# Kernel optimization log

Measured on AMD Instinct MI355X. Metric: run time of the kernel, lower is better.

The kernel has to match this reference:

```python
import jax, jax.numpy as jnp
import numpy as np

B, N, E, DIN, H1, H2, DOUT = 2, 20000, 320000, 128, 256, 256, 128


def setup_inputs() -> dict:
    key = jax.random.key(0)
    ks = jax.random.split(key, 9)
    X = jax.random.normal(ks[0], (B, N, DIN), dtype=jnp.float32)
    edge_index = jax.random.randint(ks[1], (2, E), 0, N, dtype=jnp.int32)
    def lin(k, fan_in, fan_out):
        lim = 1.0 / np.sqrt(fan_in)
        return jax.random.uniform(k, (fan_in, fan_out), jnp.float32, -lim, lim)
    W1 = lin(ks[2], DIN, H1); b1 = jnp.zeros((H1,), jnp.float32)
    W2 = lin(ks[3], H1, H2);  b2 = jnp.zeros((H2,), jnp.float32)
    W3 = lin(ks[4], H2, DOUT); b3 = jnp.zeros((DOUT,), jnp.float32)
    prelu_a = jnp.array(0.25, jnp.float32)  # PReLU default single shared param
    return dict(X=X, W1=W1, b1=b1, W2=W2, b2=b2, W3=W3, b3=b3,
                prelu_a=prelu_a, edge_index=edge_index)


def reference(X, W1, b1, W2, b2, W3, b3, prelu_a, edge_index):
    src, dst = edge_index[0], edge_index[1]
    n = X.shape[1]
    # GCN symmetric normalization with self-loops: deg = in-degree + 1
    deg = jax.ops.segment_sum(jnp.ones_like(src, X.dtype), dst, num_segments=n) + 1.0
    dinv = jax.lax.rsqrt(deg)                      # [N]
    norm_e = dinv[src] * dinv[dst]                 # [E] edge norm
    norm_self = dinv * dinv                        # [N] self-loop norm

    def gcn(x, W, b):
        h = x @ W                                  # [N, F_out]
        agg = jax.ops.segment_sum(h[src] * norm_e[:, None], dst, num_segments=n)
        agg = agg + h * norm_self[:, None]         # add self-loop message
        return agg + b

    def prelu(x):
        return jnp.where(x >= 0, x, prelu_a * x)

    def single(x):  # x: [N, DIN]
        x = prelu(gcn(x, W1, b1))
        x = prelu(gcn(x, W2, b2))
        return gcn(x, W3, b3)

    return jax.vmap(single)(X)                     # [B, N, DOUT]
```

## Files before the change

kernel.cpp:

```cpp
#include <hip/hip_runtime.h>

#define NB 20000
#define EB 320000
#define DIN 128
#define H1D 256
#define H2D 256
#define DOUTD 128
#define SCAN_BLOCKS ((NB + 255) / 256)


__global__ void zero_kernel(int* __restrict__ p, int n) {
    int t = blockIdx.x * blockDim.x + threadIdx.x;
    if (t < n) p[t] = 0;
}

__global__ void hist_kernel(const int* __restrict__ dst, int* __restrict__ bins) {
    int t = blockIdx.x * blockDim.x + threadIdx.x;
    if (t < EB) atomicAdd(&bins[dst[t]], 1);
}

__global__ __launch_bounds__(256) void scanA_kernel(const int* __restrict__ bins,
                                                    int* __restrict__ loc,
                                                    int* __restrict__ blksum) {
    __shared__ int s[256];
    int t = threadIdx.x;
    int i = blockIdx.x * 256 + t;
    int v = (i < NB) ? bins[i] : 0;
    s[t] = v;
    __syncthreads();
    for (int off = 1; off < 256; off <<= 1) {
        int u = (t >= off) ? s[t - off] : 0;
        __syncthreads();
        s[t] += u;
        __syncthreads();
    }
    if (i < NB) loc[i] = s[t] - v;
    if (t == 255) blksum[blockIdx.x] = s[255];
}

__global__ __launch_bounds__(128) void scanB_kernel(int* __restrict__ blksum) {
    __shared__ int s[128];
    int t = threadIdx.x;
    int v = (t < SCAN_BLOCKS) ? blksum[t] : 0;
    s[t] = v;
    __syncthreads();
    for (int off = 1; off < 128; off <<= 1) {
        int u = (t >= off) ? s[t - off] : 0;
        __syncthreads();
        s[t] += u;
        __syncthreads();
    }
    if (t < SCAN_BLOCKS) blksum[t] = s[t] - v;
}

__global__ __launch_bounds__(256) void scanC_kernel(const int* __restrict__ bins,
                                                    const int* __restrict__ loc,
                                                    const int* __restrict__ blksum,
                                                    int* __restrict__ rs,
                                                    int* __restrict__ cursor,
                                                    float* __restrict__ dinv) {
    int i = blockIdx.x * 256 + threadIdx.x;
    if (i < NB) {
        int r = loc[i] + blksum[blockIdx.x];
        rs[i] = r;
        cursor[i] = r;
        dinv[i] = rsqrtf((float)bins[i] + 1.0f);
    }
    if (i == 0) rs[NB] = EB;
}

__global__ void scatter_kernel(const int* __restrict__ src, const int* __restrict__ dst,
                               const float* __restrict__ dinv,
                               int* __restrict__ cursor, int2* __restrict__ edges) {
    int t = blockIdx.x * blockDim.x + threadIdx.x;
    if (t < EB) {
        int d = dst[t], s = src[t];
        int p = atomicAdd(&cursor[d], 1);
        edges[p] = make_int2(s, __float_as_int(dinv[s] * dinv[d]));
    }
}


template <int F, bool SPLIT_IN, bool SPLIT_OUT, bool BIAS, bool PRELU>
__global__ __launch_bounds__(256) void aggv_kernel(
    const float* __restrict__ h, float* __restrict__ out,
    const int* __restrict__ rs, const int2* __restrict__ edges,
    const float* __restrict__ dinv, const float* __restrict__ bias,
    const float* __restrict__ pa, int phase) {
    const int ss = blockIdx.x & 7;
    const int chunk = blockIdx.x >> 3;
    const int wid = threadIdx.x >> 6;
    const int lane = threadIdx.x & 63;
    const int li = lane & 31;
    const int eh = lane >> 5;
    const int b = ss >> 2;
    const int c32 = (ss & 3) + phase * 4;
    const int fo = c32 * 32 + li;

    constexpr size_t GS = SPLIT_IN ? F : 2 * F;
    constexpr size_t OS = SPLIT_OUT ? F : 2 * F;
    const float* gb = h + (SPLIT_IN ? (size_t)b * NB * F : (size_t)b * F) + fo;
    float* ob = out + (SPLIT_OUT ? (size_t)b * NB * F : (size_t)b * F) + fo;

    const float pav = PRELU ? *pa : 0.0f;
    const float bval = BIAS ? bias[fo] : 0.0f;

    int n = chunk * 20 + wid * 5;
    int e1n = __builtin_amdgcn_readfirstlane(rs[n]);
    for (int j = 0; j < 5; ++j, ++n) {
        int e0 = e1n;
        e1n = __builtin_amdgcn_readfirstlane(rs[n + 1]);
        int e1 = e1n;
        float a0 = 0.f, a1 = 0.f, a2 = 0.f, a3 = 0.f;
        int e = e0;
        for (; e + 8 <= e1; e += 8) {
            int2 r0 = edges[e + eh];
            int2 r1 = edges[e + 2 + eh];
            int2 r2 = edges[e + 4 + eh];
            int2 r3 = edges[e + 6 + eh];
            float t0 = gb[(size_t)r0.x * GS];
            float t1 = gb[(size_t)r1.x * GS];
            float t2 = gb[(size_t)r2.x * GS];
            float t3 = gb[(size_t)r3.x * GS];
            a0 = fmaf(t0, __int_as_float(r0.y), a0);
            a1 = fmaf(t1, __int_as_float(r1.y), a1);
            a2 = fmaf(t2, __int_as_float(r2.y), a2);
            a3 = fmaf(t3, __int_as_float(r3.y), a3);
        }
        for (; e + 2 <= e1; e += 2) {
            int2 r0 = edges[e + eh];
            a0 = fmaf(gb[(size_t)r0.x * GS], __int_as_float(r0.y), a0);
        }
        if (e < e1) {
            int my = e + eh;
            bool valid = (my < e1);
            int2 r0 = edges[valid ? my : e];
            float w = valid ? __int_as_float(r0.y) : 0.0f;
            a0 = fmaf(gb[(size_t)r0.x * GS], w, a0);
        }
        float acc = (a0 + a1) + (a2 + a3);
        acc += __shfl_xor(acc, 32, 64);
        float dv = dinv[n];
        float r = fmaf(gb[(size_t)n * GS], dv * dv, acc);
        if (BIAS) r += bval;
        if (PRELU) r = (r >= 0.0f) ? r : pav * r;
        if (eh == 0) ob[(size_t)n * OS] = r;
    }
}

template <bool BIAS, bool PRELU>
__global__ __launch_bounds__(256) void gemm_kernel(const float* __restrict__ A, int M, int K,
                                                   const float* __restrict__ W, int Nc,
                                                   const float* __restrict__ bias,
                                                   const float* __restrict__ pa,
                                                   float* __restrict__ C) {
    __shared__ alignas(16) float As[16][132];
    __shared__ alignas(16) float Bs[16][68];
    int t = threadIdx.x;
    int bm = blockIdx.x * 128;
    int bn = blockIdx.y * 64;
    int tx = t & 15, ty = t >> 4;
    int m0 = ty * 8, n0 = tx * 4;
    int ar = t >> 2, ac4 = (t & 3) * 4;
    int br = t >> 4, bc4 = (t & 15) * 4;

    float acc[8][4] = {};

    for (int k0 = 0; k0 < K; k0 += 16) {
        float4 a0 = make_float4(0.f, 0.f, 0.f, 0.f), a1 = a0;
        int r0 = bm + ar, r1 = bm + ar + 64;
        if (r0 < M) a0 = *(const float4*)&A[(size_t)r0 * K + k0 + ac4];
        if (r1 < M) a1 = *(const float4*)&A[(size_t)r1 * K + k0 + ac4];
        As[ac4 + 0][ar] = a0.x; As[ac4 + 1][ar] = a0.y;
        As[ac4 + 2][ar] = a0.z; As[ac4 + 3][ar] = a0.w;
        As[ac4 + 0][ar + 64] = a1.x; As[ac4 + 1][ar + 64] = a1.y;
        As[ac4 + 2][ar + 64] = a1.z; As[ac4 + 3][ar + 64] = a1.w;
        float4 bv = *(const float4*)&W[(size_t)(k0 + br) * Nc + bn + bc4];
        *(float4*)&Bs[br][bc4] = bv;
        __syncthreads();
#pragma unroll
        for (int k = 0; k < 16; ++k) {
            float4 av0 = *(const float4*)&As[k][m0];
            float4 av1 = *(const float4*)&As[k][m0 + 4];
            float4 bv4 = *(const float4*)&Bs[k][n0];
            float a_[8] = {av0.x, av0.y, av0.z, av0.w, av1.x, av1.y, av1.z, av1.w};
            float b_[4] = {bv4.x, bv4.y, bv4.z, bv4.w};
#pragma unroll
            for (int i = 0; i < 8; ++i)
#pragma unroll
                for (int j = 0; j < 4; ++j)
                    acc[i][j] = fmaf(a_[i], b_[j], acc[i][j]);
        }
        __syncthreads();
    }

    float pav = 0.0f;
    if (PRELU) pav = *pa;
#pragma unroll
    for (int i = 0; i < 8; ++i) {
        int row = bm + m0 + i;
        if (row < M) {
            float v[4];
#pragma unroll
            for (int j = 0; j < 4; ++j) {
                float x = acc[i][j];
                if (BIAS) x += bias[bn + n0 + j];
                if (PRELU) x = (x >= 0.0f) ? x : pav * x;
                v[j] = x;
            }
            *(float4*)&C[(size_t)row * Nc + bn + n0] = make_float4(v[0], v[1], v[2], v[3]);
        }
    }
}


static inline char* carve(char*& p, size_t bytes) {
    char* r = p;
    p += (bytes + 255) & ~(size_t)255;
    return r;
}

extern "C" void kernel_launch(void* const* d_in, const int* in_sizes, int n_in,
                              void* d_out, int out_size, void* d_ws, size_t ws_size,
                              hipStream_t stream) {
    const float* X  = (const float*)d_in[0];
    const float* W1 = (const float*)d_in[1];
    const float* b1 = (const float*)d_in[2];
    const float* W2 = (const float*)d_in[3];
    const float* b2 = (const float*)d_in[4];
    const float* W3 = (const float*)d_in[5];
    const float* b3 = (const float*)d_in[6];
    const float* pa = (const float*)d_in[7];
    const int* ei   = (const int*)d_in[8];
    const int* src = ei;
    const int* dst = ei + EB;
    float* out = (float*)d_out;

    char* p = (char*)d_ws;
    int* bins    = (int*)carve(p, NB * sizeof(int));
    int* loc     = (int*)carve(p, NB * sizeof(int));
    int* blksum  = (int*)carve(p, 128 * sizeof(int));
    int* rs      = (int*)carve(p, (NB + 1) * sizeof(int));
    int* cursor  = (int*)carve(p, NB * sizeof(int));
    int2* edges  = (int2*)carve(p, EB * sizeof(int2));
    float* dinv  = (float*)carve(p, NB * sizeof(float));
    float* bufA  = (float*)carve(p, (size_t)2 * NB * 256 * sizeof(float));
    float* bufB  = (float*)carve(p, (size_t)2 * NB * 256 * sizeof(float));

    const int M = 2 * NB;
    const int AGGV = 1000 * 8;

    zero_kernel<<<SCAN_BLOCKS, 256, 0, stream>>>(bins, NB);
    hist_kernel<<<(EB + 255) / 256, 256, 0, stream>>>(dst, bins);
    scanA_kernel<<<SCAN_BLOCKS, 256, 0, stream>>>(bins, loc, blksum);
    scanB_kernel<<<1, 128, 0, stream>>>(blksum);
    scanC_kernel<<<SCAN_BLOCKS, 256, 0, stream>>>(bins, loc, blksum, rs, cursor, dinv);
    scatter_kernel<<<(EB + 255) / 256, 256, 0, stream>>>(src, dst, dinv, cursor, edges);

    aggv_kernel<128, true, false, false, false><<<AGGV, 256, 0, stream>>>(
        X, bufA, rs, edges, dinv, nullptr, nullptr, 0);

    gemm_kernel<true, true><<<dim3((M + 127) / 128, H1D / 64), 256, 0, stream>>>(
        bufA, M, DIN, W1, H1D, b1, pa, bufB);

    gemm_kernel<false, false><<<dim3((M + 127) / 128, H2D / 64), 256, 0, stream>>>(
        bufB, M, H1D, W2, H2D, nullptr, nullptr, bufA);

    aggv_kernel<256, false, false, true, true><<<AGGV, 256, 0, stream>>>(
        bufA, bufB, rs, edges, dinv, b2, pa, 0);
    aggv_kernel<256, false, false, true, true><<<AGGV, 256, 0, stream>>>(
        bufA, bufB, rs, edges, dinv, b2, pa, 1);

    gemm_kernel<false, false><<<dim3((M + 127) / 128, DOUTD / 64), 256, 0, stream>>>(
        bufB, M, H2D, W3, DOUTD, nullptr, nullptr, bufA);

    aggv_kernel<128, false, true, true, false><<<AGGV, 256, 0, stream>>>(
        bufA, out, rs, edges, dinv, b3, nullptr, 0);
}
```

Baseline: 490.7 us.

## Pipeline the two batches so GEMM and aggregation blocks share launches

Splits the two batch elements into separate per-batch buffers and staggers them. Each launch then runs the GEMM tiles of one batch alongside the sparse aggregation blocks of the other, so compute-bound and gather-bound work overlap. The GEMM also gains register prefetch of the next k-tile and nontemporal loads and stores in the fused variant. This adds launch-level complexity and depends on how the hardware scheduler interleaves the heterogeneous blocks. Block dispatch order could still leave either side as a tail.

```diff
diff --git a/kernel.cpp b/kernel.cpp
--- a/kernel.cpp
+++ b/kernel.cpp
@@ -7,6 +7,27 @@
 #define H2D 256
 #define DOUTD 128
 #define SCAN_BLOCKS ((NB + 255) / 256)
+#define MT 157
+
+typedef __attribute__((ext_vector_type(4))) float fvec4;
+
+template <bool NT>
+__device__ inline float4 ld4(const float* p) {
+    if (NT) {
+        fvec4 v = __builtin_nontemporal_load((const fvec4*)p);
+        return make_float4(v.x, v.y, v.z, v.w);
+    }
+    return *(const float4*)p;
+}
+template <bool NT>
+__device__ inline void st4(float* p, float4 v) {
+    if (NT) {
+        fvec4 t; t.x = v.x; t.y = v.y; t.z = v.z; t.w = v.w;
+        __builtin_nontemporal_store(t, (fvec4*)p);
+    } else {
+        *(float4*)p = v;
+    }
+}
 
 
 __global__ void zero_kernel(int* __restrict__ p, int n) {
@@ -81,31 +102,29 @@
 }
 
 
-template <int F, bool SPLIT_IN, bool SPLIT_OUT, bool BIAS, bool PRELU>
-__global__ __launch_bounds__(256) void aggv_kernel(
-    const float* __restrict__ h, float* __restrict__ out,
-    const int* __restrict__ rs, const int2* __restrict__ edges,
-    const float* __restrict__ dinv, const float* __restrict__ bias,
-    const float* __restrict__ pa, int phase) {
-    const int ss = blockIdx.x & 7;
-    const int chunk = blockIdx.x >> 3;
+template <int F, bool BIAS, bool PRELU>
+__device__ void aggv_body(int a, int ss,
+                          const float* __restrict__ h, float* __restrict__ out,
+                          const int* __restrict__ rs, const int2* __restrict__ edges,
+                          const float* __restrict__ dinv, const float* __restrict__ bias,
+                          const float* __restrict__ pa) {
+    constexpr int NS = F / 32;
+    constexpr int NH = 8 / NS;
+    const int half = (NH == 2) ? (ss >> 2) : 0;
+    const int c32 = ss & (NS - 1);
+    const int chunk = a >> 3;
     const int wid = threadIdx.x >> 6;
     const int lane = threadIdx.x & 63;
     const int li = lane & 31;
     const int eh = lane >> 5;
-    const int b = ss >> 2;
-    const int c32 = (ss & 3) + phase * 4;
     const int fo = c32 * 32 + li;
 
-    constexpr size_t GS = SPLIT_IN ? F : 2 * F;
-    constexpr size_t OS = SPLIT_OUT ? F : 2 * F;
-    const float* gb = h + (SPLIT_IN ? (size_t)b * NB * F : (size_t)b * F) + fo;
-    float* ob = out + (SPLIT_OUT ? (size_t)b * NB * F : (size_t)b * F) + fo;
-
+    const float* gb = h + fo;
+    float* ob = out + fo;
     const float pav = PRELU ? *pa : 0.0f;
     const float bval = BIAS ? bias[fo] : 0.0f;
 
-    int n = chunk * 20 + wid * 5;
+    int n = half * (NB / NH) + chunk * 20 + wid * 5;
     int e1n = __builtin_amdgcn_readfirstlane(rs[n]);
     for (int j = 0; j < 5; ++j, ++n) {
         int e0 = e1n;
@@ -118,10 +137,10 @@
             int2 r1 = edges[e + 2 + eh];
             int2 r2 = edges[e + 4 + eh];
             int2 r3 = edges[e + 6 + eh];
-            float t0 = gb[(size_t)r0.x * GS];
-            float t1 = gb[(size_t)r1.x * GS];
-            float t2 = gb[(size_t)r2.x * GS];
-            float t3 = gb[(size_t)r3.x * GS];
+            float t0 = gb[(size_t)r0.x * F];
+            float t1 = gb[(size_t)r1.x * F];
+            float t2 = gb[(size_t)r2.x * F];
+            float t3 = gb[(size_t)r3.x * F];
             a0 = fmaf(t0, __int_as_float(r0.y), a0);
             a1 = fmaf(t1, __int_as_float(r1.y), a1);
             a2 = fmaf(t2, __int_as_float(r2.y), a2);
@@ -129,55 +148,65 @@
         }
         for (; e + 2 <= e1; e += 2) {
             int2 r0 = edges[e + eh];
-            a0 = fmaf(gb[(size_t)r0.x * GS], __int_as_float(r0.y), a0);
+            a0 = fmaf(gb[(size_t)r0.x * F], __int_as_float(r0.y), a0);
         }
         if (e < e1) {
             int my = e + eh;
             bool valid = (my < e1);
             int2 r0 = edges[valid ? my : e];
             float w = valid ? __int_as_float(r0.y) : 0.0f;
-            a0 = fmaf(gb[(size_t)r0.x * GS], w, a0);
+            a0 = fmaf(gb[(size_t)r0.x * F], w, a0);
         }
         float acc = (a0 + a1) + (a2 + a3);
         acc += __shfl_xor(acc, 32, 64);
         float dv = dinv[n];
-        float r = fmaf(gb[(size_t)n * GS], dv * dv, acc);
+        float r = fmaf(gb[(size_t)n * F], dv * dv, acc);
         if (BIAS) r += bval;
         if (PRELU) r = (r >= 0.0f) ? r : pav * r;
-        if (eh == 0) ob[(size_t)n * OS] = r;
-    }
-}
-
-template <bool BIAS, bool PRELU>
-__global__ __launch_bounds__(256) void gemm_kernel(const float* __restrict__ A, int M, int K,
-                                                   const float* __restrict__ W, int Nc,
-                                                   const float* __restrict__ bias,
-                                                   const float* __restrict__ pa,
-                                                   float* __restrict__ C) {
+        if (eh == 0) ob[(size_t)n * F] = r;
+    }
+}
+
+template <bool BIAS, bool PRELU, bool NT>
+__device__ void gemm_body(int gx, const float* __restrict__ A, int K,
+                          const float* __restrict__ W, int Nc,
+                          const float* __restrict__ bias, const float* __restrict__ pa,
+                          float* __restrict__ C) {
     __shared__ alignas(16) float As[16][132];
     __shared__ alignas(16) float Bs[16][68];
+    const int M = NB;
     int t = threadIdx.x;
-    int bm = blockIdx.x * 128;
-    int bn = blockIdx.y * 64;
+    int bm = (gx % MT) * 128;
+    int bn = (gx / MT) * 64;
     int tx = t & 15, ty = t >> 4;
     int m0 = ty * 8, n0 = tx * 4;
     int ar = t >> 2, ac4 = (t & 3) * 4;
     int br = t >> 4, bc4 = (t & 15) * 4;
+    int r0 = bm + ar, r1 = bm + ar + 64;
+    bool v0 = r0 < M, v1 = r1 < M;
+    const float* pA0 = A + (size_t)r0 * K + ac4;
+    const float* pA1 = A + (size_t)r1 * K + ac4;
+    const float* pW = W + (size_t)br * Nc + bn + bc4;
+
+    float4 a0 = make_float4(0.f, 0.f, 0.f, 0.f), a1 = a0;
+    if (v0) a0 = ld4<NT>(pA0);
+    if (v1) a1 = ld4<NT>(pA1);
+    float4 bv = *(const float4*)pW;
 
     float acc[8][4] = {};
 
     for (int k0 = 0; k0 < K; k0 += 16) {
-        float4 a0 = make_float4(0.f, 0.f, 0.f, 0.f), a1 = a0;
-        int r0 = bm + ar, r1 = bm + ar + 64;
-        if (r0 < M) a0 = *(const float4*)&A[(size_t)r0 * K + k0 + ac4];
-        if (r1 < M) a1 = *(const float4*)&A[(size_t)r1 * K + k0 + ac4];
         As[ac4 + 0][ar] = a0.x; As[ac4 + 1][ar] = a0.y;
         As[ac4 + 2][ar] = a0.z; As[ac4 + 3][ar] = a0.w;
         As[ac4 + 0][ar + 64] = a1.x; As[ac4 + 1][ar + 64] = a1.y;
         As[ac4 + 2][ar + 64] = a1.z; As[ac4 + 3][ar + 64] = a1.w;
-        float4 bv = *(const float4*)&W[(size_t)(k0 + br) * Nc + bn + bc4];
         *(float4*)&Bs[br][bc4] = bv;
         __syncthreads();
+        if (k0 + 16 < K) {
+            a0 = v0 ? ld4<NT>(pA0 + k0 + 16) : make_float4(0.f, 0.f, 0.f, 0.f);
+            a1 = v1 ? ld4<NT>(pA1 + k0 + 16) : make_float4(0.f, 0.f, 0.f, 0.f);
+            bv = *(const float4*)(pW + (size_t)(k0 + 16) * Nc);
+        }
 #pragma unroll
         for (int k = 0; k < 16; ++k) {
             float4 av0 = *(const float4*)&As[k][m0];
@@ -208,9 +237,48 @@
                 if (PRELU) x = (x >= 0.0f) ? x : pav * x;
                 v[j] = x;
             }
-            *(float4*)&C[(size_t)row * Nc + bn + n0] = make_float4(v[0], v[1], v[2], v[3]);
-        }
-    }
+            st4<NT>(&C[(size_t)row * Nc + bn + n0], make_float4(v[0], v[1], v[2], v[3]));
+        }
+    }
+}
+
+
+template <int F, bool BIAS, bool PRELU>
+__global__ __launch_bounds__(256) void aggv_kernel(
+    const float* __restrict__ h, float* __restrict__ out,
+    const int* __restrict__ rs, const int2* __restrict__ edges,
+    const float* __restrict__ dinv, const float* __restrict__ bias,
+    const float* __restrict__ pa) {
+    aggv_body<F, BIAS, PRELU>(blockIdx.x, blockIdx.x & 7, h, out, rs, edges,
+                              dinv, bias, pa);
+}
+
+template <int AF, bool AB, bool AP, bool GB_, bool GP>
+__global__ __launch_bounds__(256) void fat_kernel(
+    const float* __restrict__ A, int K, const float* __restrict__ W, int Nc,
+    const float* __restrict__ gbias, float* __restrict__ C, int ng,
+    const float* __restrict__ ah, float* __restrict__ aout,
+    const int* __restrict__ rs, const int2* __restrict__ edges,
+    const float* __restrict__ dinv, const float* __restrict__ abias,
+    const float* __restrict__ pa) {
+    int bx = blockIdx.x;
+    if (bx < ng) {
+        gemm_body<GB_, GP, true>(bx, A, K, W, Nc, gbias, pa, C);
+    } else {
+        aggv_body<AF, AB, AP>(bx - ng, bx & 7, ah, aout, rs, edges, dinv, abias, pa);
+    }
+}
+
+template <bool B1, bool P1, bool B2, bool P2>
+__global__ __launch_bounds__(256) void gemm2_kernel(
+    const float* __restrict__ A1p, int K1, const float* __restrict__ W1p, int N1,
+    const float* __restrict__ bias1, float* __restrict__ C1, int ng1,
+    const float* __restrict__ A2p, int K2, const float* __restrict__ W2p, int N2,
+    const float* __restrict__ bias2, float* __restrict__ C2,
+    const float* __restrict__ pa) {
+    int bx = blockIdx.x;
+    if (bx < ng1) gemm_body<B1, P1, false>(bx, A1p, K1, W1p, N1, bias1, pa, C1);
+    else          gemm_body<B2, P2, false>(bx - ng1, A2p, K2, W2p, N2, bias2, pa, C2);
 }
 
 
@@ -244,11 +312,15 @@
     int* cursor  = (int*)carve(p, NB * sizeof(int));
     int2* edges  = (int2*)carve(p, EB * sizeof(int2));
     float* dinv  = (float*)carve(p, NB * sizeof(float));
-    float* bufA  = (float*)carve(p, (size_t)2 * NB * 256 * sizeof(float));
-    float* bufB  = (float*)carve(p, (size_t)2 * NB * 256 * sizeof(float));
-
-    const int M = 2 * NB;
-    const int AGGV = 1000 * 8;
+    float* P0 = (float*)carve(p, (size_t)NB * 256 * sizeof(float));
+    float* Q0 = (float*)carve(p, (size_t)NB * 256 * sizeof(float));
+    float* P1 = (float*)carve(p, (size_t)NB * 256 * sizeof(float));
+    float* Q1 = (float*)carve(p, (size_t)NB * 256 * sizeof(float));
+
+    const float* X0 = X;
+    const float* X1 = X + (size_t)NB * DIN;
+    float* out0 = out;
+    float* out1 = out + (size_t)NB * DOUTD;
 
     zero_kernel<<<SCAN_BLOCKS, 256, 0, stream>>>(bins, NB);
     hist_kernel<<<(EB + 255) / 256, 256, 0, stream>>>(dst, bins);
@@ -257,23 +329,35 @@
     scanC_kernel<<<SCAN_BLOCKS, 256, 0, stream>>>(bins, loc, blksum, rs, cursor, dinv);
     scatter_kernel<<<(EB + 255) / 256, 256, 0, stream>>>(src, dst, dinv, cursor, edges);
 
-    aggv_kernel<128, true, false, false, false><<<AGGV, 256, 0, stream>>>(
-        X, bufA, rs, edges, dinv, nullptr, nullptr, 0);
-
-    gemm_kernel<true, true><<<dim3((M + 127) / 128, H1D / 64), 256, 0, stream>>>(
-        bufA, M, DIN, W1, H1D, b1, pa, bufB);
-
-    gemm_kernel<false, false><<<dim3((M + 127) / 128, H2D / 64), 256, 0, stream>>>(
-        bufB, M, H1D, W2, H2D, nullptr, nullptr, bufA);
-
-    aggv_kernel<256, false, false, true, true><<<AGGV, 256, 0, stream>>>(
-        bufA, bufB, rs, edges, dinv, b2, pa, 0);
-    aggv_kernel<256, false, false, true, true><<<AGGV, 256, 0, stream>>>(
-        bufA, bufB, rs, edges, dinv, b2, pa, 1);
-
-    gemm_kernel<false, false><<<dim3((M + 127) / 128, DOUTD / 64), 256, 0, stream>>>(
-        bufB, M, H2D, W3, DOUTD, nullptr, nullptr, bufA);
-
-    aggv_kernel<128, false, true, true, false><<<AGGV, 256, 0, stream>>>(
-        bufA, out, rs, edges, dinv, b3, nullptr, 0);
-}
+    const int NA128 = 4000;
+    const int NA256 = 8000;
+    const int NG256 = MT * 4;
+    const int NG128 = MT * 2;
+
+
+    aggv_kernel<128, false, false><<<NA128, 256, 0, stream>>>(
+        X0, P0, rs, edges, dinv, nullptr, nullptr);
+
+    fat_kernel<128, false, false, true, true><<<NG256 + NA128, 256, 0, stream>>>(
+        P0, DIN, W1, H1D, b1, Q0, NG256,
+        X1, P1, rs, edges, dinv, nullptr, pa);
+
+    gemm2_kernel<false, false, true, true><<<NG256 + NG256, 256, 0, stream>>>(
+        Q0, H1D, W2, H2D, nullptr, P0, NG256,
+        P1, DIN, W1, H1D, b1, Q1, pa);
+
+    fat_kernel<256, true, true, false, false><<<NG256 + NA256, 256, 0, stream>>>(
+        Q1, H1D, W2, H2D, nullptr, P1, NG256,
+        P0, Q0, rs, edges, dinv, b2, pa);
+
+    fat_kernel<256, true, true, false, false><<<NG128 + NA256, 256, 0, stream>>>(
+        Q0, H2D, W3, DOUTD, nullptr, P0, NG128,
+        P1, Q1, rs, edges, dinv, b2, pa);
+
+    fat_kernel<128, true, false, false, false><<<NG128 + NA128, 256, 0, stream>>>(
+        Q1, H2D, W3, DOUTD, nullptr, P1, NG128,
+        P0, out0, rs, edges, dinv, b3, pa);
+
+    aggv_kernel<128, true, false><<<NA128, 256, 0, stream>>>(
+        P1, out1, rs, edges, dinv, b3, nullptr);
+}
```

After: 788.1 us. +60.6%, slower.

## Replace FP32 SIMT GEMMs with split-bf16 MFMA GEMMs

Applied to the files above, without the earlier changes.

Swaps the scalar FP32 tiled GEMM for a matrix-core GEMM that uses bf16 MFMA instructions. Precision is kept by splitting each operand into high and low bf16 parts and summing three products (hh, hl, lh). Activations feeding the GEMMs are written as hi/lo bf16 pairs by the aggregation and GEMM epilogues, and the weights are converted and transposed by a new small kernel. This adds three extra launches and triples the MFMA work in exchange for matrix-core throughput, and it risks a small accuracy loss against the FP32 reference.

```diff
diff --git a/kernel.cpp b/kernel.cpp
--- a/kernel.cpp
+++ b/kernel.cpp
@@ -7,6 +7,18 @@
 #define H2D 256
 #define DOUTD 128
 #define SCAN_BLOCKS ((NB + 255) / 256)
+
+typedef __attribute__((ext_vector_type(8))) short short8;
+typedef __attribute__((ext_vector_type(4))) float f32x4;
+
+__device__ inline void bsplit(float x, unsigned short& h, unsigned short& l) {
+    unsigned u = __float_as_uint(x);
+    unsigned hr = (u + 0x7FFFu + ((u >> 16) & 1u)) & 0xFFFF0000u;
+    h = (unsigned short)(hr >> 16);
+    float lo = x - __uint_as_float(hr);
+    unsigned v = __float_as_uint(lo);
+    l = (unsigned short)((v + 0x7FFFu + ((v >> 16) & 1u)) >> 16);
+}
 
 
 __global__ void zero_kernel(int* __restrict__ p, int n) {
@@ -80,10 +92,24 @@
     }
 }
 
-
-template <int F, bool SPLIT_IN, bool SPLIT_OUT, bool BIAS, bool PRELU>
+__global__ void wcvt_kernel(const float* __restrict__ W,
+                            unsigned short* __restrict__ Wth,
+                            unsigned short* __restrict__ Wtl, int K, int Nc) {
+    int i = blockIdx.x * 256 + threadIdx.x;
+    if (i < K * Nc) {
+        int k = i / Nc, n = i % Nc;
+        unsigned short h, l;
+        bsplit(W[i], h, l);
+        Wth[(size_t)n * K + k] = h;
+        Wtl[(size_t)n * K + k] = l;
+    }
+}
+
+
+template <int F, bool SPLIT_IN, bool SPLIT_OUT, bool BIAS, bool PRELU, int OUT>
 __global__ __launch_bounds__(256) void aggv_kernel(
     const float* __restrict__ h, float* __restrict__ out,
+    unsigned short* __restrict__ oh, unsigned short* __restrict__ ol,
     const int* __restrict__ rs, const int2* __restrict__ edges,
     const float* __restrict__ dinv, const float* __restrict__ bias,
     const float* __restrict__ pa, int phase) {
@@ -100,7 +126,15 @@
     constexpr size_t GS = SPLIT_IN ? F : 2 * F;
     constexpr size_t OS = SPLIT_OUT ? F : 2 * F;
     const float* gb = h + (SPLIT_IN ? (size_t)b * NB * F : (size_t)b * F) + fo;
-    float* ob = out + (SPLIT_OUT ? (size_t)b * NB * F : (size_t)b * F) + fo;
+    float* ob = nullptr;
+    unsigned short* ohb = nullptr;
+    unsigned short* olb = nullptr;
+    if (OUT == 0) {
+        ob = out + (SPLIT_OUT ? (size_t)b * NB * F : (size_t)b * F) + fo;
+    } else {
+        ohb = oh + (size_t)b * F + fo;
+        olb = ol + (size_t)b * F + fo;
+    }
 
     const float pav = PRELU ? *pa : 0.0f;
     const float bval = BIAS ? bias[fo] : 0.0f;
@@ -144,71 +178,109 @@
         float r = fmaf(gb[(size_t)n * GS], dv * dv, acc);
         if (BIAS) r += bval;
         if (PRELU) r = (r >= 0.0f) ? r : pav * r;
-        if (eh == 0) ob[(size_t)n * OS] = r;
-    }
-}
-
-template <bool BIAS, bool PRELU>
-__global__ __launch_bounds__(256) void gemm_kernel(const float* __restrict__ A, int M, int K,
-                                                   const float* __restrict__ W, int Nc,
-                                                   const float* __restrict__ bias,
-                                                   const float* __restrict__ pa,
-                                                   float* __restrict__ C) {
-    __shared__ alignas(16) float As[16][132];
-    __shared__ alignas(16) float Bs[16][68];
-    int t = threadIdx.x;
-    int bm = blockIdx.x * 128;
-    int bn = blockIdx.y * 64;
-    int tx = t & 15, ty = t >> 4;
-    int m0 = ty * 8, n0 = tx * 4;
-    int ar = t >> 2, ac4 = (t & 3) * 4;
-    int br = t >> 4, bc4 = (t & 15) * 4;
-
-    float acc[8][4] = {};
-
-    for (int k0 = 0; k0 < K; k0 += 16) {
-        float4 a0 = make_float4(0.f, 0.f, 0.f, 0.f), a1 = a0;
-        int r0 = bm + ar, r1 = bm + ar + 64;
-        if (r0 < M) a0 = *(const float4*)&A[(size_t)r0 * K + k0 + ac4];
-        if (r1 < M) a1 = *(const float4*)&A[(size_t)r1 * K + k0 + ac4];
-        As[ac4 + 0][ar] = a0.x; As[ac4 + 1][ar] = a0.y;
-        As[ac4 + 2][ar] = a0.z; As[ac4 + 3][ar] = a0.w;
-        As[ac4 + 0][ar + 64] = a1.x; As[ac4 + 1][ar + 64] = a1.y;
-        As[ac4 + 2][ar + 64] = a1.z; As[ac4 + 3][ar + 64] = a1.w;
-        float4 bv = *(const float4*)&W[(size_t)(k0 + br) * Nc + bn + bc4];
-        *(float4*)&Bs[br][bc4] = bv;
-        __syncthreads();
-#pragma unroll
-        for (int k = 0; k < 16; ++k) {
-            float4 av0 = *(const float4*)&As[k][m0];
-            float4 av1 = *(const float4*)&As[k][m0 + 4];
-            float4 bv4 = *(const float4*)&Bs[k][n0];
-            float a_[8] = {av0.x, av0.y, av0.z, av0.w, av1.x, av1.y, av1.z, av1.w};
-            float b_[4] = {bv4.x, bv4.y, bv4.z, bv4.w};
-#pragma unroll
-            for (int i = 0; i < 8; ++i)
-#pragma unroll
-                for (int j = 0; j < 4; ++j)
-                    acc[i][j] = fmaf(a_[i], b_[j], acc[i][j]);
-        }
-        __syncthreads();
-    }
-
-    float pav = 0.0f;
-    if (PRELU) pav = *pa;
-#pragma unroll
-    for (int i = 0; i < 8; ++i) {
-        int row = bm + m0 + i;
-        if (row < M) {
-            float v[4];
+        if (eh == 0) {
+            if (OUT == 0) {
+                ob[(size_t)n * OS] = r;
+            } else {
+                unsigned short hh, ll;
+                bsplit(r, hh, ll);
+                ohb[(size_t)n * 2 * F] = hh;
+                olb[(size_t)n * 2 * F] = ll;
+            }
+        }
+    }
+}
+
+template <bool BIAS, bool PRELU, int OM>
+__global__ __launch_bounds__(256) void gemmb_kernel(
+    const unsigned short* __restrict__ Ah, const unsigned short* __restrict__ Al, int K,
+    const unsigned short* __restrict__ Wth, const unsigned short* __restrict__ Wtl, int Nc,
+    const float* __restrict__ bias, const float* __restrict__ pa,
+    float* __restrict__ C, unsigned short* __restrict__ Ch, unsigned short* __restrict__ Cl) {
+    const int M = 2 * NB;
+    __shared__ unsigned short Ash[128][40];
+    __shared__ unsigned short Asl[128][40];
+    __shared__ unsigned short Bsh[64][40];
+    __shared__ unsigned short Bsl[64][40];
+
+    const int t = threadIdx.x;
+    const int bm = blockIdx.x * 128;
+    const int bn = blockIdx.y * 64;
+    const int w = t >> 6;
+    const int l = t & 63;
+    const int lm = l & 15;
+    const int lk = (l >> 4) * 8;
+
+    f32x4 acc[2][4];
+#pragma unroll
+    for (int m = 0; m < 2; ++m)
+#pragma unroll
+        for (int nt = 0; nt < 4; ++nt) acc[m][nt] = (f32x4){0.f, 0.f, 0.f, 0.f};
+
+    for (int k0 = 0; k0 < K; k0 += 32) {
+#pragma unroll
+        for (int i = 0; i < 2; ++i) {
+            int c = t + i * 256;
+            int row = c >> 2, seg = (c & 3) * 8;
+            int gr = bm + row;
+            short8 vh = (short8){0, 0, 0, 0, 0, 0, 0, 0};
+            short8 vl = vh;
+            if (gr < M) {
+                vh = *(const short8*)&Ah[(size_t)gr * K + k0 + seg];
+                vl = *(const short8*)&Al[(size_t)gr * K + k0 + seg];
+            }
+            *(short8*)&Ash[row][seg] = vh;
+            *(short8*)&Asl[row][seg] = vl;
+        }
+        {
+            int n = t >> 2, seg = (t & 3) * 8;
+            *(short8*)&Bsh[n][seg] = *(const short8*)&Wth[(size_t)(bn + n) * K + k0 + seg];
+            *(short8*)&Bsl[n][seg] = *(const short8*)&Wtl[(size_t)(bn + n) * K + k0 + seg];
+        }
+        __syncthreads();
+
+        short8 ah0 = *(const short8*)&Ash[w * 32 + lm][lk];
+        short8 ah1 = *(const short8*)&Ash[w * 32 + 16 + lm][lk];
+        short8 al0 = *(const short8*)&Asl[w * 32 + lm][lk];
+        short8 al1 = *(const short8*)&Asl[w * 32 + 16 + lm][lk];
+#pragma unroll
+        for (int nt = 0; nt < 4; ++nt) {
+            short8 bh = *(const short8*)&Bsh[nt * 16 + lm][lk];
+            short8 bl = *(const short8*)&Bsl[nt * 16 + lm][lk];
+            acc[0][nt] = __builtin_amdgcn_mfma_f32_16x16x32_bf16(ah0, bh, acc[0][nt], 0, 0, 0);
+            acc[0][nt] = __builtin_amdgcn_mfma_f32_16x16x32_bf16(ah0, bl, acc[0][nt], 0, 0, 0);
+            acc[0][nt] = __builtin_amdgcn_mfma_f32_16x16x32_bf16(al0, bh, acc[0][nt], 0, 0, 0);
+            acc[1][nt] = __builtin_amdgcn_mfma_f32_16x16x32_bf16(ah1, bh, acc[1][nt], 0, 0, 0);
+            acc[1][nt] = __builtin_amdgcn_mfma_f32_16x16x32_bf16(ah1, bl, acc[1][nt], 0, 0, 0);
+            acc[1][nt] = __builtin_amdgcn_mfma_f32_16x16x32_bf16(al1, bh, acc[1][nt], 0, 0, 0);
+        }
+        __syncthreads();
+    }
+
+    const float pav = PRELU ? *pa : 0.0f;
+    const int lg = l >> 4;
+#pragma unroll
+    for (int m = 0; m < 2; ++m) {
+#pragma unroll
+        for (int nt = 0; nt < 4; ++nt) {
+            int col = bn + nt * 16 + lm;
+            float bv = BIAS ? bias[col] : 0.0f;
 #pragma unroll
             for (int j = 0; j < 4; ++j) {
-                float x = acc[i][j];
-                if (BIAS) x += bias[bn + n0 + j];
-                if (PRELU) x = (x >= 0.0f) ? x : pav * x;
-                v[j] = x;
+                int row = bm + w * 32 + m * 16 + lg * 4 + j;
+                if (row < M) {
+                    float r = acc[m][nt][j] + bv;
+                    if (PRELU) r = (r >= 0.0f) ? r : pav * r;
+                    if (OM == 0) {
+                        C[(size_t)row * Nc + col] = r;
+                    } else {
+                        unsigned short hh, ll;
+                        bsplit(r, hh, ll);
+                        Ch[(size_t)row * Nc + col] = hh;
+                        Cl[(size_t)row * Nc + col] = ll;
+                    }
+                }
             }
-            *(float4*)&C[(size_t)row * Nc + bn + n0] = make_float4(v[0], v[1], v[2], v[3]);
         }
     }
 }
@@ -244,11 +316,24 @@
     int* cursor  = (int*)carve(p, NB * sizeof(int));
     int2* edges  = (int2*)carve(p, EB * sizeof(int2));
     float* dinv  = (float*)carve(p, NB * sizeof(float));
-    float* bufA  = (float*)carve(p, (size_t)2 * NB * 256 * sizeof(float));
-    float* bufB  = (float*)carve(p, (size_t)2 * NB * 256 * sizeof(float));
+    unsigned short* W1th = (unsigned short*)carve(p, DIN * H1D * 2);
+    unsigned short* W1tl = (unsigned short*)carve(p, DIN * H1D * 2);
+    unsigned short* W2th = (unsigned short*)carve(p, H1D * H2D * 2);
+    unsigned short* W2tl = (unsigned short*)carve(p, H1D * H2D * 2);
+    unsigned short* W3th = (unsigned short*)carve(p, H2D * DOUTD * 2);
+    unsigned short* W3tl = (unsigned short*)carve(p, H2D * DOUTD * 2);
+    char* U = carve(p, (size_t)2 * NB * 256 * sizeof(float));
+    char* V = carve(p, (size_t)2 * NB * 256 * sizeof(float));
 
     const int M = 2 * NB;
-    const int AGGV = 1000 * 8;
+    unsigned short* A1h = (unsigned short*)U;
+    unsigned short* A1l = A1h + (size_t)M * DIN;
+    float* R = (float*)U;
+    float* T = (float*)U;
+    unsigned short* G1h = (unsigned short*)V;
+    unsigned short* G1l = G1h + (size_t)M * H1D;
+    unsigned short* Sh = (unsigned short*)V;
+    unsigned short* Sl = Sh + (size_t)M * H2D;
 
     zero_kernel<<<SCAN_BLOCKS, 256, 0, stream>>>(bins, NB);
     hist_kernel<<<(EB + 255) / 256, 256, 0, stream>>>(dst, bins);
@@ -256,24 +341,30 @@
     scanB_kernel<<<1, 128, 0, stream>>>(blksum);
     scanC_kernel<<<SCAN_BLOCKS, 256, 0, stream>>>(bins, loc, blksum, rs, cursor, dinv);
     scatter_kernel<<<(EB + 255) / 256, 256, 0, stream>>>(src, dst, dinv, cursor, edges);
-
-    aggv_kernel<128, true, false, false, false><<<AGGV, 256, 0, stream>>>(
-        X, bufA, rs, edges, dinv, nullptr, nullptr, 0);
-
-    gemm_kernel<true, true><<<dim3((M + 127) / 128, H1D / 64), 256, 0, stream>>>(
-        bufA, M, DIN, W1, H1D, b1, pa, bufB);
-
-    gemm_kernel<false, false><<<dim3((M + 127) / 128, H2D / 64), 256, 0, stream>>>(
-        bufB, M, H1D, W2, H2D, nullptr, nullptr, bufA);
-
-    aggv_kernel<256, false, false, true, true><<<AGGV, 256, 0, stream>>>(
-        bufA, bufB, rs, edges, dinv, b2, pa, 0);
-    aggv_kernel<256, false, false, true, true><<<AGGV, 256, 0, stream>>>(
-        bufA, bufB, rs, edges, dinv, b2, pa, 1);
-
-    gemm_kernel<false, false><<<dim3((M + 127) / 128, DOUTD / 64), 256, 0, stream>>>(
-        bufB, M, H2D, W3, DOUTD, nullptr, nullptr, bufA);
-
-    aggv_kernel<128, false, true, true, false><<<AGGV, 256, 0, stream>>>(
-        bufA, out, rs, edges, dinv, b3, nullptr, 0);
-}
+    wcvt_kernel<<<(DIN * H1D + 255) / 256, 256, 0, stream>>>(W1, W1th, W1tl, DIN, H1D);
+    wcvt_kernel<<<(H1D * H2D + 255) / 256, 256, 0, stream>>>(W2, W2th, W2tl, H1D, H2D);
+    wcvt_kernel<<<(H2D * DOUTD + 255) / 256, 256, 0, stream>>>(W3, W3th, W3tl, H2D, DOUTD);
+
+    const int AGGV = 8000;
+    const int MT2 = (M + 127) / 128;
+
+    aggv_kernel<128, true, false, false, false, 1><<<AGGV, 256, 0, stream>>>(
+        X, nullptr, A1h, A1l, rs, edges, dinv, nullptr, nullptr, 0);
+
+    gemmb_kernel<true, true, 1><<<dim3(MT2, H1D / 64), 256, 0, stream>>>(
+        A1h, A1l, DIN, W1th, W1tl, H1D, b1, pa, nullptr, G1h, G1l);
+
+    gemmb_kernel<false, false, 0><<<dim3(MT2, H2D / 64), 256, 0, stream>>>(
+        G1h, G1l, H1D, W2th, W2tl, H2D, nullptr, nullptr, R, nullptr, nullptr);
+
+    aggv_kernel<256, false, false, true, true, 1><<<AGGV, 256, 0, stream>>>(
+        R, nullptr, Sh, Sl, rs, edges, dinv, b2, pa, 0);
+    aggv_kernel<256, false, false, true, true, 1><<<AGGV, 256, 0, stream>>>(
+        R, nullptr, Sh, Sl, rs, edges, dinv, b2, pa, 1);
+
+    gemmb_kernel<false, false, 0><<<dim3(MT2, DOUTD / 64), 256, 0, stream>>>(
+        Sh, Sl, H2D, W3th, W3tl, DOUTD, nullptr, nullptr, T, nullptr, nullptr);
+
+    aggv_kernel<128, false, true, true, false, 0><<<AGGV, 256, 0, stream>>>(
+        T, out, nullptr, nullptr, rs, edges, dinv, b3, nullptr, 0);
+}
```

After: 442.1 us. 9.9% less time.
